# Kernel optimization log

Measured on AMD Instinct MI355X. Metric: run time of the kernel, lower is better.

## Reference

```python
import jax, jax.numpy as jnp
import numpy as np

N = 50000   # nodes
E = 800000  # edges
V = 10000   # vocab
D = 128     # emb_dim
H = 128     # hidden_dim
C = 10      # num_classes
G = 512     # graphs in batch


def setup_inputs() -> dict:
    key = jax.random.key(0)
    ks = jax.random.split(key, 10)
    return {
        "x_tokens": jax.random.randint(ks[0], (N,), 0, V),
        "edge_index": jax.random.randint(ks[1], (2, E), 0, N),
        "batch": jnp.sort(jax.random.randint(ks[2], (N,), 0, G)),
        "emb": jax.random.normal(ks[3], (V, D), dtype=jnp.float32) * 0.05,
        "w1": jax.random.normal(ks[4], (D, H), dtype=jnp.float32) * 0.05,
        "b1": jax.random.normal(ks[5], (H,), dtype=jnp.float32) * 0.05,
        "w2": jax.random.normal(ks[6], (H, H), dtype=jnp.float32) * 0.05,
        "b2": jax.random.normal(ks[7], (H,), dtype=jnp.float32) * 0.05,
        "lin_w": jax.random.normal(ks[8], (H, C), dtype=jnp.float32) * 0.05,
        "lin_b": jax.random.normal(ks[9], (C,), dtype=jnp.float32) * 0.05,
    }


def _gcn_conv(x, W, b, src, dst, norm):
    # PyG GCNConv: x' = D^{-1/2}(A+I)D^{-1/2} X W + b (self-loops already in src/dst)
    h = x @ W                                  # [N, H]
    msg = h[src] * norm[:, None]               # [E+N, H] gather + scale
    return jax.ops.segment_sum(msg, dst, num_segments=N) + b


def reference(x_tokens, edge_index, batch, emb, w1, b1, w2, b2, lin_w, lin_b):
    # embedding with padding_idx=0 (row 0 forced to zero)
    table = emb * (jnp.arange(V) != 0)[:, None].astype(emb.dtype)
    x = table[x_tokens]                        # [N, D]

    # add self loops, symmetric degree normalization (computed once)
    loops = jnp.arange(N)
    src = jnp.concatenate([edge_index[0], loops])
    dst = jnp.concatenate([edge_index[1], loops])
    deg = jax.ops.segment_sum(jnp.ones_like(dst, dtype=x.dtype), dst, num_segments=N)
    dis = jax.lax.rsqrt(deg)                   # deg >= 1 due to self loops
    norm = dis[src] * dis[dst]                 # [E+N]

    x = jax.nn.relu(_gcn_conv(x, w1, b1, src, dst, norm))
    x = jax.nn.relu(_gcn_conv(x, w2, b2, src, dst, norm))

    # global mean pool over graphs
    sums = jax.ops.segment_sum(x, batch, num_segments=G)          # [G, H]
    cnts = jax.ops.segment_sum(jnp.ones((N,), x.dtype), batch, num_segments=G)
    pooled = sums / jnp.maximum(cnts, 1.0)[:, None]

    return pooled @ lin_w + lin_b              # [G, C]
```

## Files before the change

### kernel.cpp

```cpp
#include <hip/hip_runtime.h>
#include <hip/hip_bf16.h>


typedef unsigned int uint;
typedef unsigned short ushort;
typedef __attribute__((ext_vector_type(8))) short bf16x8;
typedef __attribute__((ext_vector_type(4))) float f32x4;

__device__ inline float bf_lo(uint u) { return __uint_as_float(u << 16); }
__device__ inline float bf_hi(uint u) { return __uint_as_float(u & 0xffff0000u); }
__device__ inline ushort f2bf(float f) {
    uint u = __float_as_uint(f);
    return (ushort)((u + 0x7fffu + ((u >> 16) & 1u)) >> 16);
}
__device__ inline uint pack2bf(float a, float b) {
    return (uint)f2bf(a) | ((uint)f2bf(b) << 16);
}

#define EPB 2048
#define CAP 8192

__global__ __launch_bounds__(256) void init0(int* __restrict__ bcur,
                                             const float* __restrict__ W1,
                                             const float* __restrict__ W2,
                                             ushort* __restrict__ W1t,
                                             ushort* __restrict__ W2t) {
    if (blockIdx.x == 0) {
        bcur[threadIdx.x] = 0;
    } else {
        int i = (blockIdx.x - 1) * 256 + threadIdx.x;
        const float* Ws = (i < 16384) ? W1 : W2;
        ushort* Wd      = (i < 16384) ? W1t : W2t;
        int j = i & 16383;
        int nn = j >> 7, k = j & 127;
        Wd[j] = f2bf(Ws[k * 128 + nn]);
    }
}

__device__ void scatter_body(int* lds,
                             const int* __restrict__ src,
                             const int* __restrict__ dst,
                             int* __restrict__ bcur,
                             uint* __restrict__ bstage,
                             int E, int NB, int bid) {
    int*  lh    = lds;
    int*  lbase = lds + 256;
    int*  gbase = lds + 513;
    int*  lcur  = lds + 769;
    int*  ls    = lds + 1025;
    uint* stage = (uint*)(lds + 1284);
    const int t = threadIdx.x;
    const int base = bid * EPB;
    const int end  = min(E, base + EPB);
    const int tot  = end - base;

    lh[t] = 0;
    __syncthreads();

    uint pk[8]; int bk[8]; int cnt = 0;
    for (int i = base + t; i < end; i += 256) {
        int s = src[i];
        uint d = (uint)dst[i];
        bk[cnt] = (int)(d >> 8);
        pk[cnt] = (uint)s | ((d & 255u) << 24);
        atomicAdd(&lh[bk[cnt]], 1);
        ++cnt;
    }
    __syncthreads();

    if (t < NB && lh[t]) gbase[t] = t * CAP + atomicAdd(&bcur[t], lh[t]);
    {
        int v = lh[t];
        ls[t] = v;
        __syncthreads();
        for (int off = 1; off < 256; off <<= 1) {
            int x = (t >= off) ? ls[t - off] : 0;
            __syncthreads();
            ls[t] += x;
            __syncthreads();
        }
        lbase[t] = ls[t] - v;
        if (t == 255) lbase[256] = ls[255];
        lcur[t] = 0;
    }
    __syncthreads();

    for (int j = 0; j < cnt; ++j) {
        int p = lbase[bk[j]] + atomicAdd(&lcur[bk[j]], 1);
        stage[p] = pk[j];
    }
    __syncthreads();

    for (int i = t; i < tot; i += 256) {
        int lo = 0, hi = 256;
        while (lo + 1 < hi) {
            int mid = (lo + hi) >> 1;
            if (lbase[mid] <= i) lo = mid; else hi = mid;
        }
        bstage[gbase[lo] + (i - lbase[lo])] = stage[i];
    }
}

__device__ void csr_body(int* lds,
                         const uint* __restrict__ bstage,
                         const int* __restrict__ bcur,
                         float* __restrict__ dis,
                         int* __restrict__ rbeg,
                         int* __restrict__ rend,
                         int* __restrict__ csr,
                         int N, int b) {
    int* lh    = lds;
    int* ls    = lds + 256;
    int* lbase = lds + 512;
    int* lcur  = lds + 768;
    const int t = threadIdx.x;
    const int base  = b * CAP;
    const int cntb  = bcur[b];
    const int n0    = b << 8;
    const int nn    = min(256, N - n0);

    lh[t] = 0;
    __syncthreads();
    for (int i = t; i < cntb; i += 256)
        atomicAdd(&lh[bstage[base + i] >> 24], 1);
    __syncthreads();

    const int v = lh[t];
    ls[t] = v;
    __syncthreads();
    for (int off = 1; off < 256; off <<= 1) {
        int x = (t >= off) ? ls[t - off] : 0;
        __syncthreads();
        ls[t] += x;
        __syncthreads();
    }
    lbase[t] = ls[t] - v;
    lcur[t] = 0;
    if (t < nn) {
        dis[n0 + t]  = rsqrtf((float)v + 1.0f);
        rbeg[n0 + t] = base + lbase[t];
        rend[n0 + t] = base + lbase[t] + v;
    }
    __syncthreads();

    for (int i = t; i < cntb; i += 256) {
        uint e = bstage[base + i];
        int dl = (int)(e >> 24);
        int pos = base + lbase[dl] + atomicAdd(&lcur[dl], 1);
        csr[pos] = (int)(e & 0xFFFFFFu);
    }
}

template<bool GATHER, bool SCALE>
__device__ void gemm_body(ushort* wl,
                          const ushort* __restrict__ Xbf,
                          const int* __restrict__ tokens,
                          const float* __restrict__ emb,
                          const ushort* __restrict__ Wt,
                          const float* __restrict__ dis,
                          ushort* __restrict__ Out, int n, int bid) {
    const int tid = threadIdx.x;
    {
        const int row  = tid >> 1;
        const int half = tid & 1;
        const int base = row * 256 + half * 128;
#pragma unroll
        for (int i = 0; i < 8; ++i) {
            int off = base + i * 16;
            uint4 v = *(const uint4*)((const char*)Wt + off);
            int swz = off ^ ((row & 7) << 4);
            *(uint4*)((char*)wl + swz) = v;
        }
    }
    __syncthreads();

    const int w  = tid >> 6;
    const int l  = tid & 63;
    const int lr = l & 15;
    const int lg = l >> 4;
    const int rowBase = bid * 128 + w * 32;

    f32x4 acc[2][8];
#pragma unroll
    for (int s = 0; s < 2; ++s)
#pragma unroll
        for (int ct = 0; ct < 8; ++ct) acc[s][ct] = (f32x4){0.f, 0.f, 0.f, 0.f};

    bf16x8 afrag[2][4];
#pragma unroll
    for (int s = 0; s < 2; ++s) {
        const int row = rowBase + s * 16 + lr;
        if (row < n) {
            if (GATHER) {
                const int tok = tokens[row];
                if (tok != 0) {
                    const float* ep = emb + (size_t)tok * 128;
#pragma unroll
                    for (int kk = 0; kk < 4; ++kk) {
                        const float* q = ep + kk * 32 + lg * 8;
                        float4 lo = *(const float4*)q;
                        float4 hi = *(const float4*)(q + 4);
                        uint4 pk;
                        pk.x = pack2bf(lo.x, lo.y); pk.y = pack2bf(lo.z, lo.w);
                        pk.z = pack2bf(hi.x, hi.y); pk.w = pack2bf(hi.z, hi.w);
                        union { uint4 u; bf16x8 b; } c; c.u = pk;
                        afrag[s][kk] = c.b;
                    }
                } else {
#pragma unroll
                    for (int kk = 0; kk < 4; ++kk) afrag[s][kk] = (bf16x8){0,0,0,0,0,0,0,0};
                }
            } else {
                const ushort* xp = Xbf + (size_t)row * 128;
#pragma unroll
                for (int kk = 0; kk < 4; ++kk)
                    afrag[s][kk] = *(const bf16x8*)(xp + kk * 32 + lg * 8);
            }
        } else {
#pragma unroll
            for (int kk = 0; kk < 4; ++kk) afrag[s][kk] = (bf16x8){0,0,0,0,0,0,0,0};
        }
    }

#pragma unroll
    for (int ct = 0; ct < 8; ++ct) {
#pragma unroll
        for (int kk = 0; kk < 4; ++kk) {
            const int nrow = ct * 16 + lr;
            int off = nrow * 256 + kk * 64 + lg * 16;
            off ^= ((nrow & 7) << 4);
            bf16x8 b = *(const bf16x8*)((const char*)wl + off);
            acc[0][ct] = __builtin_amdgcn_mfma_f32_16x16x32_bf16(afrag[0][kk], b, acc[0][ct], 0, 0, 0);
            acc[1][ct] = __builtin_amdgcn_mfma_f32_16x16x32_bf16(afrag[1][kk], b, acc[1][ct], 0, 0, 0);
        }
    }

#pragma unroll
    for (int s = 0; s < 2; ++s) {
#pragma unroll
        for (int r = 0; r < 4; ++r) {
            const int row = rowBase + s * 16 + lg * 4 + r;
            if (row < n) {
                const float sc = SCALE ? dis[row] : 1.0f;
                ushort* op = Out + (size_t)row * 128 + lr;
#pragma unroll
                for (int ct = 0; ct < 8; ++ct)
                    op[ct * 16] = f2bf(acc[s][ct][r] * sc);
            }
        }
    }
}

__global__ __launch_bounds__(256) void scatter_gemm1_fused(const int* __restrict__ src,
                                                           const int* __restrict__ dst,
                                                           int* __restrict__ bcur,
                                                           uint* __restrict__ bstage,
                                                           const int* __restrict__ tokens,
                                                           const float* __restrict__ emb,
                                                           const ushort* __restrict__ W1t,
                                                           ushort* __restrict__ H,
                                                           int E, int NB, int EB, int N) {
    __shared__ ushort wl[128 * 128];
    const int b = blockIdx.x;
    if (b < EB) {
        scatter_body((int*)wl, src, dst, bcur, bstage, E, NB, b);
    } else {
        gemm_body<true, false>(wl, nullptr, tokens, emb, W1t, nullptr, H, N, b - EB);
    }
}

__global__ __launch_bounds__(256) void csr_poolz(const uint* __restrict__ bstage,
                                                 const int* __restrict__ bcur,
                                                 float* __restrict__ dis,
                                                 int* __restrict__ rbeg,
                                                 int* __restrict__ rend,
                                                 int* __restrict__ csr,
                                                 int4* __restrict__ poolz, int pz4,
                                                 int N, int NB) {
    __shared__ int lds[1024];
    const int b = blockIdx.x;
    if (b < NB) {
        csr_body(lds, bstage, bcur, dis, rbeg, rend, csr, N, b);
    } else {
        int i = (b - NB) * 256 + threadIdx.x;
        if (i < pz4) poolz[i] = make_int4(0, 0, 0, 0);
    }
}

__global__ __launch_bounds__(256) void agg1_gemm2(const ushort* __restrict__ H,
                                                  const float* __restrict__ dis,
                                                  const int* __restrict__ rbeg,
                                                  const int* __restrict__ rend,
                                                  const int* __restrict__ csr,
                                                  const float* __restrict__ bias,
                                                  const ushort* __restrict__ W2t,
                                                  ushort* __restrict__ Hs2,
                                                  int n) {
    const int g = threadIdx.x >> 4;
    const int l = threadIdx.x & 15;
    const int node = blockIdx.x * 16 + g;
    const bool valid = node < n;

    float s0_=0.f,s1_=0.f,s2_=0.f,s3_=0.f,s4_=0.f,s5_=0.f,s6_=0.f,s7_=0.f;
    float dn = 0.f;
    const float4 bA = *(const float4*)&bias[l * 8];
    const float4 bB = *(const float4*)&bias[l * 8 + 4];
    float hx0=0.f,hx1=0.f,hx2=0.f,hx3=0.f,hx4=0.f,hx5=0.f,hx6=0.f,hx7=0.f;

    if (valid) {
        dn = dis[node];
        const uint4 hq = *(const uint4*)(H + (size_t)node * 128 + l * 8);
        hx0 = bf_lo(hq.x); hx1 = bf_hi(hq.x);
        hx2 = bf_lo(hq.y); hx3 = bf_hi(hq.y);
        hx4 = bf_lo(hq.z); hx5 = bf_hi(hq.z);
        hx6 = bf_lo(hq.w); hx7 = bf_hi(hq.w);

        const int e0 = rbeg[node];
        const int e1 = rend[node];
        int e = e0;
        for (; e + 8 <= e1; e += 8) {
            int a[8];
#pragma unroll
            for (int j = 0; j < 8; ++j) a[j] = csr[e + j];
            float w[8];
#pragma unroll
            for (int j = 0; j < 8; ++j) w[j] = dis[a[j]];
            uint4 h[8];
#pragma unroll
            for (int j = 0; j < 8; ++j) h[j] = *(const uint4*)(H + (size_t)a[j] * 128 + l * 8);
#pragma unroll
            for (int j = 0; j < 8; ++j) {
                s0_ += bf_lo(h[j].x) * w[j]; s1_ += bf_hi(h[j].x) * w[j];
                s2_ += bf_lo(h[j].y) * w[j]; s3_ += bf_hi(h[j].y) * w[j];
                s4_ += bf_lo(h[j].z) * w[j]; s5_ += bf_hi(h[j].z) * w[j];
                s6_ += bf_lo(h[j].w) * w[j]; s7_ += bf_hi(h[j].w) * w[j];
            }
        }
        for (; e + 4 <= e1; e += 4) {
            int a[4];
#pragma unroll
            for (int j = 0; j < 4; ++j) a[j] = csr[e + j];
            float w[4];
#pragma unroll
            for (int j = 0; j < 4; ++j) w[j] = dis[a[j]];
            uint4 h[4];
#pragma unroll
            for (int j = 0; j < 4; ++j) h[j] = *(const uint4*)(H + (size_t)a[j] * 128 + l * 8);
#pragma unroll
            for (int j = 0; j < 4; ++j) {
                s0_ += bf_lo(h[j].x) * w[j]; s1_ += bf_hi(h[j].x) * w[j];
                s2_ += bf_lo(h[j].y) * w[j]; s3_ += bf_hi(h[j].y) * w[j];
                s4_ += bf_lo(h[j].z) * w[j]; s5_ += bf_hi(h[j].z) * w[j];
                s6_ += bf_lo(h[j].w) * w[j]; s7_ += bf_hi(h[j].w) * w[j];
            }
        }
        for (; e < e1; ++e) {
            const int a = csr[e];
            const float w = dis[a];
            const uint4 h = *(const uint4*)(H + (size_t)a * 128 + l * 8);
            s0_ += bf_lo(h.x)*w; s1_ += bf_hi(h.x)*w;
            s2_ += bf_lo(h.y)*w; s3_ += bf_hi(h.y)*w;
            s4_ += bf_lo(h.z)*w; s5_ += bf_hi(h.z)*w;
            s6_ += bf_lo(h.w)*w; s7_ += bf_hi(h.w)*w;
        }
    }

    const float self = dn * dn;
    uint4 o;
    o.x = pack2bf(fmaxf(s0_ * dn + hx0 * self + bA.x, 0.0f),
                  fmaxf(s1_ * dn + hx1 * self + bA.y, 0.0f));
    o.y = pack2bf(fmaxf(s2_ * dn + hx2 * self + bA.z, 0.0f),
                  fmaxf(s3_ * dn + hx3 * self + bA.w, 0.0f));
    o.z = pack2bf(fmaxf(s4_ * dn + hx4 * self + bB.x, 0.0f),
                  fmaxf(s5_ * dn + hx5 * self + bB.y, 0.0f));
    o.w = pack2bf(fmaxf(s6_ * dn + hx6 * self + bB.z, 0.0f),
                  fmaxf(s7_ * dn + hx7 * self + bB.w, 0.0f));

    __shared__ ushort x2[16 * 128];
    {
        int boff = (g << 8) + (l << 4);
        boff ^= (g & 7) << 4;
        *(uint4*)((char*)x2 + boff) = o;
    }
    __syncthreads();

    const int w   = threadIdx.x >> 6;
    const int l64 = threadIdx.x & 63;
    const int lr  = l64 & 15;
    const int lg  = l64 >> 4;

    bf16x8 afr[4];
#pragma unroll
    for (int kk = 0; kk < 4; ++kk) {
        int roff = (lr << 8) + (kk << 6) + (lg << 4);
        roff ^= (lr & 7) << 4;
        afr[kk] = *(const bf16x8*)((const char*)x2 + roff);
    }

    f32x4 acc[2];
    acc[0] = (f32x4){0.f, 0.f, 0.f, 0.f};
    acc[1] = (f32x4){0.f, 0.f, 0.f, 0.f};
#pragma unroll
    for (int ci = 0; ci < 2; ++ci) {
        const int ct = (w << 1) | ci;
#pragma unroll
        for (int kk = 0; kk < 4; ++kk) {
            bf16x8 b = *(const bf16x8*)(W2t + (size_t)(ct * 16 + lr) * 128 + kk * 32 + lg * 8);
            acc[ci] = __builtin_amdgcn_mfma_f32_16x16x32_bf16(afr[kk], b, acc[ci], 0, 0, 0);
        }
    }

#pragma unroll
    for (int r = 0; r < 4; ++r) {
        const int row = blockIdx.x * 16 + lg * 4 + r;
        if (row < n) {
            const float sc = dis[row];
            ushort* op = Hs2 + (size_t)row * 128 + lr;
            op[(w * 2) * 16]     = f2bf(acc[0][r] * sc);
            op[(w * 2 + 1) * 16] = f2bf(acc[1][r] * sc);
        }
    }
}

__global__ __launch_bounds__(256) void aggregate_pool(const ushort* __restrict__ H,
                                                      const float* __restrict__ dis,
                                                      const int* __restrict__ rbeg,
                                                      const int* __restrict__ rend,
                                                      const int* __restrict__ csr,
                                                      const float* __restrict__ bias,
                                                      const int* __restrict__ batch,
                                                      float* __restrict__ pooled,
                                                      int n) {
    const int g = threadIdx.x >> 4;
    const int l = threadIdx.x & 15;
    const int node = blockIdx.x * 16 + g;
    const bool valid = node < n;

    float s0_=0.f,s1_=0.f,s2_=0.f,s3_=0.f,s4_=0.f,s5_=0.f,s6_=0.f,s7_=0.f;
    float dn = 0.f;
    const float4 bA = *(const float4*)&bias[l * 8];
    const float4 bB = *(const float4*)&bias[l * 8 + 4];

    if (valid) {
        dn = dis[node];
        const uint4 hq = *(const uint4*)(H + (size_t)node * 128 + l * 8);
        s0_ = bf_lo(hq.x); s1_ = bf_hi(hq.x);
        s2_ = bf_lo(hq.y); s3_ = bf_hi(hq.y);
        s4_ = bf_lo(hq.z); s5_ = bf_hi(hq.z);
        s6_ = bf_lo(hq.w); s7_ = bf_hi(hq.w);

        const int e0 = rbeg[node];
        const int e1 = rend[node];
        int e = e0;
        for (; e + 8 <= e1; e += 8) {
            int a[8];
#pragma unroll
            for (int j = 0; j < 8; ++j) a[j] = csr[e + j];
            uint4 h[8];
#pragma unroll
            for (int j = 0; j < 8; ++j) h[j] = *(const uint4*)(H + (size_t)a[j] * 128 + l * 8);
#pragma unroll
            for (int j = 0; j < 8; ++j) {
                s0_ += bf_lo(h[j].x); s1_ += bf_hi(h[j].x);
                s2_ += bf_lo(h[j].y); s3_ += bf_hi(h[j].y);
                s4_ += bf_lo(h[j].z); s5_ += bf_hi(h[j].z);
                s6_ += bf_lo(h[j].w); s7_ += bf_hi(h[j].w);
            }
        }
        for (; e + 4 <= e1; e += 4) {
            int a[4];
#pragma unroll
            for (int j = 0; j < 4; ++j) a[j] = csr[e + j];
            uint4 h[4];
#pragma unroll
            for (int j = 0; j < 4; ++j) h[j] = *(const uint4*)(H + (size_t)a[j] * 128 + l * 8);
#pragma unroll
            for (int j = 0; j < 4; ++j) {
                s0_ += bf_lo(h[j].x); s1_ += bf_hi(h[j].x);
                s2_ += bf_lo(h[j].y); s3_ += bf_hi(h[j].y);
                s4_ += bf_lo(h[j].z); s5_ += bf_hi(h[j].z);
                s6_ += bf_lo(h[j].w); s7_ += bf_hi(h[j].w);
            }
        }
        for (; e < e1; ++e) {
            const uint4 h = *(const uint4*)(H + (size_t)csr[e] * 128 + l * 8);
            s0_ += bf_lo(h.x); s1_ += bf_hi(h.x);
            s2_ += bf_lo(h.y); s3_ += bf_hi(h.y);
            s4_ += bf_lo(h.z); s5_ += bf_hi(h.z);
            s6_ += bf_lo(h.w); s7_ += bf_hi(h.w);
        }
    }

    const float o0 = fmaxf(s0_ * dn + bA.x, 0.0f);
    const float o1 = fmaxf(s1_ * dn + bA.y, 0.0f);
    const float o2 = fmaxf(s2_ * dn + bA.z, 0.0f);
    const float o3 = fmaxf(s3_ * dn + bA.w, 0.0f);
    const float o4 = fmaxf(s4_ * dn + bB.x, 0.0f);
    const float o5 = fmaxf(s5_ * dn + bB.y, 0.0f);
    const float o6 = fmaxf(s6_ * dn + bB.z, 0.0f);
    const float o7 = fmaxf(s7_ * dn + bB.w, 0.0f);

    __shared__ float x3[16][128];
    __shared__ int bv[16];
    if (valid) {
        float4 va, vb;
        va.x = o0; va.y = o1; va.z = o2; va.w = o3;
        vb.x = o4; vb.y = o5; vb.z = o6; vb.w = o7;
        *(float4*)&x3[g][l * 8]     = va;
        *(float4*)&x3[g][l * 8 + 4] = vb;
        if (l == 0) bv[g] = batch[node];
    } else if (l == 0) {
        bv[g] = -1;
    }
    __syncthreads();
    const int t = threadIdx.x;
    if (t < 128) {
        int cur = bv[0];
        float run = 0.0f;
        for (int r = 0; r < 16; ++r) {
            const int b = bv[r];
            if (b < 0) break;
            if (b != cur) {
                if (run != 0.0f) atomicAdd(&pooled[(size_t)cur * 128 + t], run);
                cur = b; run = 0.0f;
            }
            run += x3[r][t];
        }
        if (cur >= 0 && run != 0.0f) atomicAdd(&pooled[(size_t)cur * 128 + t], run);
    }
}

__global__ __launch_bounds__(128) void pool_finalize(const float* __restrict__ pooled,
                                                     const int* __restrict__ batch,
                                                     const float* __restrict__ lw,
                                                     const float* __restrict__ lb,
                                                     float* __restrict__ out, int n) {
    const int g = blockIdx.x;
    const int t = threadIdx.x;
    int lo = 0, hi = n;
    while (lo < hi) { int mid = (lo + hi) >> 1; if (batch[mid] < g) lo = mid + 1; else hi = mid; }
    const int s = lo;
    hi = n;
    while (lo < hi) { int mid = (lo + hi) >> 1; if (batch[mid] < g + 1) lo = mid + 1; else hi = mid; }
    const float c = fmaxf((float)(lo - s), 1.0f);

    __shared__ float pl[128];
    pl[t] = pooled[(size_t)g * 128 + t] / c;
    __syncthreads();
    if (t < 10) {
        float acc = lb[t];
#pragma unroll 16
        for (int d = 0; d < 128; ++d) acc += pl[d] * lw[d * 10 + t];
        out[g * 10 + t] = acc;
    }
}

extern "C" void kernel_launch(void* const* d_in, const int* in_sizes, int n_in,
                              void* d_out, int out_size, void* d_ws, size_t ws_size,
                              hipStream_t stream) {
    const int*   tokens = (const int*)d_in[0];
    const int*   eidx   = (const int*)d_in[1];
    const int*   batch  = (const int*)d_in[2];
    const float* emb    = (const float*)d_in[3];
    const float* w1     = (const float*)d_in[4];
    const float* b1     = (const float*)d_in[5];
    const float* w2     = (const float*)d_in[6];
    const float* b2     = (const float*)d_in[7];
    const float* lw     = (const float*)d_in[8];
    const float* lbv    = (const float*)d_in[9];

    const int N = in_sizes[0];
    const int E = in_sizes[1] / 2;
    const int G = out_size / 10;
    const int* src = eidx;
    const int* dst = eidx + E;
    const int NB = (N + 255) >> 8;
    const int GB = (N + 127) / 128;

    char* p = (char*)d_ws;
    auto alloc = [&](size_t bytes) { void* r = (void*)p; p += (bytes + 255) & ~(size_t)255; return r; };
    float*  dis    = (float*)alloc((size_t)N * 4);
    int*    rbeg   = (int*)  alloc((size_t)N * 4);
    int*    rend   = (int*)  alloc((size_t)N * 4);
    int*    bcur   = (int*)  alloc(256 * 4);
    float*  pooled = (float*)alloc((size_t)G * 128 * 4);
    uint*   bstage = (uint*) alloc((size_t)NB * CAP * 4);
    int*    csr    = (int*)  alloc((size_t)NB * CAP * 4);
    ushort* W1t    = (ushort*)alloc(16384 * 2);
    ushort* W2t    = (ushort*)alloc(16384 * 2);
    ushort* A      = (ushort*)alloc((size_t)N * 128 * 2);
    ushort* B      = (ushort*)alloc((size_t)N * 128 * 2);

    const int PZ4 = (G * 128) / 4;
    const int PZB = (PZ4 + 255) / 256;
    const int EB  = (E + EPB - 1) / EPB;

    init0<<<129, 256, 0, stream>>>(bcur, w1, w2, W1t, W2t);
    scatter_gemm1_fused<<<EB + GB, 256, 0, stream>>>(src, dst, bcur, bstage,
                                                     tokens, emb, W1t, A, E, NB, EB, N);
    csr_poolz<<<NB + PZB, 256, 0, stream>>>(bstage, bcur, dis, rbeg, rend, csr,
                                            (int4*)pooled, PZ4, N, NB);
    agg1_gemm2<<<(N + 15) / 16, 256, 0, stream>>>(A, dis, rbeg, rend, csr, b1, W2t, B, N);
    aggregate_pool<<<(N + 15) / 16, 256, 0, stream>>>(B, dis, rbeg, rend, csr, b2, batch, pooled, N);
    pool_finalize<<<G, 128, 0, stream>>>(pooled, batch, lw, lbv, (float*)d_out, N);
}
```

Before: 132.7 us.

## Sort nodes by degree within each bucket to balance first aggregation

Inside the CSR-building blocks, each 256-node bucket now gets a counting sort of its nodes by in-degree, and the result is stored in a permutation array. agg1_gemm2 processes nodes in that permuted order, so the 16 nodes grouped into one block have similar degree, which reduces load imbalance across wavefronts in the gather loop. In exchange it adds an extra sort with several barriers in csr_poolz, an indirection load, scattered output row writes, and padding blocks for out-of-range entries.

```diff
diff --git a/kernel.cpp b/kernel.cpp
--- a/kernel.cpp
+++ b/kernel.cpp
@@ -108,6 +108,7 @@
                          int* __restrict__ rbeg,
                          int* __restrict__ rend,
                          int* __restrict__ csr,
+                         int* __restrict__ perm,
                          int N, int b) {
     int* lh    = lds;
     int* ls    = lds + 256;
@@ -148,6 +149,29 @@
         int dl = (int)(e >> 24);
         int pos = base + lbase[dl] + atomicAdd(&lcur[dl], 1);
         csr[pos] = (int)(e & 0xFFFFFFu);
+    }
+
+    __syncthreads();
+    perm[n0 + t] = 0x7FFFFFFF;
+    lh[t] = 0;
+    __syncthreads();
+    const int bin = min(v, 255);
+    if (t < nn) atomicAdd(&lh[bin], 1);
+    __syncthreads();
+    ls[t] = lh[t];
+    __syncthreads();
+    for (int off = 1; off < 256; off <<= 1) {
+        int x = (t >= off) ? ls[t - off] : 0;
+        __syncthreads();
+        ls[t] += x;
+        __syncthreads();
+    }
+    lbase[t] = ls[t] - lh[t];
+    lcur[t] = 0;
+    __syncthreads();
+    if (t < nn) {
+        int p = lbase[bin] + atomicAdd(&lcur[bin], 1);
+        perm[n0 + p] = n0 + t;
     }
 }
 
@@ -275,12 +299,13 @@
                                                  int* __restrict__ rbeg,
                                                  int* __restrict__ rend,
                                                  int* __restrict__ csr,
+                                                 int* __restrict__ perm,
                                                  int4* __restrict__ poolz, int pz4,
                                                  int N, int NB) {
     __shared__ int lds[1024];
     const int b = blockIdx.x;
     if (b < NB) {
-        csr_body(lds, bstage, bcur, dis, rbeg, rend, csr, N, b);
+        csr_body(lds, bstage, bcur, dis, rbeg, rend, csr, perm, N, b);
     } else {
         int i = (b - NB) * 256 + threadIdx.x;
         if (i < pz4) poolz[i] = make_int4(0, 0, 0, 0);
@@ -294,11 +319,12 @@
                                                   const int* __restrict__ csr,
                                                   const float* __restrict__ bias,
                                                   const ushort* __restrict__ W2t,
+                                                  const int* __restrict__ perm,
                                                   ushort* __restrict__ Hs2,
                                                   int n) {
     const int g = threadIdx.x >> 4;
     const int l = threadIdx.x & 15;
-    const int node = blockIdx.x * 16 + g;
+    const int node = perm[blockIdx.x * 16 + g];
     const bool valid = node < n;
 
     float s0_=0.f,s1_=0.f,s2_=0.f,s3_=0.f,s4_=0.f,s5_=0.f,s6_=0.f,s7_=0.f;
@@ -412,7 +438,7 @@
 
 #pragma unroll
     for (int r = 0; r < 4; ++r) {
-        const int row = blockIdx.x * 16 + lg * 4 + r;
+        const int row = perm[blockIdx.x * 16 + lg * 4 + r];
         if (row < n) {
             const float sc = dis[row];
             ushort* op = Hs2 + (size_t)row * 128 + lr;
@@ -583,6 +609,7 @@
     int*    rbeg   = (int*)  alloc((size_t)N * 4);
     int*    rend   = (int*)  alloc((size_t)N * 4);
     int*    bcur   = (int*)  alloc(256 * 4);
+    int*    perm   = (int*)  alloc((size_t)NB * 256 * 4);
     float*  pooled = (float*)alloc((size_t)G * 128 * 4);
     uint*   bstage = (uint*) alloc((size_t)NB * CAP * 4);
     int*    csr    = (int*)  alloc((size_t)NB * CAP * 4);
@@ -599,8 +626,8 @@
     scatter_gemm1_fused<<<EB + GB, 256, 0, stream>>>(src, dst, bcur, bstage,
                                                      tokens, emb, W1t, A, E, NB, EB, N);
     csr_poolz<<<NB + PZB, 256, 0, stream>>>(bstage, bcur, dis, rbeg, rend, csr,
-                                            (int4*)pooled, PZ4, N, NB);
-    agg1_gemm2<<<(N + 15) / 16, 256, 0, stream>>>(A, dis, rbeg, rend, csr, b1, W2t, B, N);
+                                            perm, (int4*)pooled, PZ4, N, NB);
+    agg1_gemm2<<<NB * 16, 256, 0, stream>>>(A, dis, rbeg, rend, csr, b1, W2t, perm, B, N);
     aggregate_pool<<<(N + 15) / 16, 256, 0, stream>>>(B, dis, rbeg, rend, csr, b2, batch, pooled, N);
     pool_finalize<<<G, 128, 0, stream>>>(pooled, batch, lw, lbv, (float*)d_out, N);
 }
```

Result: slower. 139.5 us (+5.1%).
